# Kernel optimization log

Measured on AMD Instinct MI355X. Metric: run time of the kernel, lower is better.

The kernel has to match this reference:

```python
import jax, jax.numpy as jnp
import numpy as np

# PlatonicConv (graph mode, attention=True, use_key=True): tetrahedron group G=12
G = 12
H_EFF = 2          # num_heads // G = 24 // 12
HEAD_D = 16        # embed_dim_g // H_EFF = (384//12) // 2
GH = G * H_EFF     # 24
IN_C = 384
EMB = 384
OUT_C = 384
N_GRAPHS = 32
NODES_PER_GRAPH = 64
N = N_GRAPHS * NODES_PER_GRAPH   # 2048
SPATIAL = 3


def _fc_edges():
    # fully-connected edges within each graph (batch[src]==batch[dst]), incl. self loops
    n = NODES_PER_GRAPH
    offs = np.arange(N_GRAPHS, dtype=np.int32) * n
    gs, gd = np.meshgrid(np.arange(n, dtype=np.int32), np.arange(n, dtype=np.int32), indexing='ij')
    src = (offs[:, None] + gs.reshape(-1)[None, :]).reshape(-1)
    dst = (offs[:, None] + gd.reshape(-1)[None, :]).reshape(-1)
    return jnp.asarray(src), jnp.asarray(dst)


def setup_inputs() -> dict:
    key = jax.random.key(0)
    ks = jax.random.split(key, 12)
    sw = 1.0 / np.sqrt(IN_C)
    x = jax.random.normal(ks[0], (N, IN_C), jnp.float32)
    pos = jax.random.normal(ks[1], (N, SPATIAL), jnp.float32)
    Wq = jax.random.normal(ks[2], (IN_C, EMB), jnp.float32) * sw
    bq = jnp.zeros((EMB,), jnp.float32)
    Wk = jax.random.normal(ks[3], (IN_C, EMB), jnp.float32) * sw
    bk = jnp.zeros((EMB,), jnp.float32)
    Wv = jax.random.normal(ks[4], (IN_C, EMB), jnp.float32) * sw
    bv = jnp.zeros((EMB,), jnp.float32)
    Wo = jax.random.normal(ks[5], (EMB, OUT_C), jnp.float32) * (1.0 / np.sqrt(EMB))
    bo = jnp.zeros((OUT_C,), jnp.float32)
    # RoPE frequencies: freq_sigma=1.0, random init, per spatial dim / head / half-dim
    rope_freqs = jax.random.normal(ks[6], (SPATIAL, H_EFF, HEAD_D // 2), jnp.float32)
    src, dst = _fc_edges()
    return {"x": x, "pos": pos, "Wq": Wq, "bq": bq, "Wk": Wk, "bk": bk,
            "Wv": Wv, "bv": bv, "Wo": Wo, "bo": bo, "rope_freqs": rope_freqs,
            "src": src, "dst": dst}


def _rope(t, pos, freqs):
    # t: [N, G, H, D]; pos: [N, 3]; freqs: [3, H, D//2]
    theta = jnp.einsum('ns,shf->nhf', pos, freqs)            # [N, H, D/2]
    cos = jnp.cos(theta)[:, None, :, :]                      # broadcast over G
    sin = jnp.sin(theta)[:, None, :, :]
    tr = t.reshape(t.shape[:-1] + (HEAD_D // 2, 2))
    t1, t2 = tr[..., 0], tr[..., 1]
    rot = jnp.stack([t1 * cos - t2 * sin, t1 * sin + t2 * cos], axis=-1)
    return rot.reshape(t.shape)


def reference(x, pos, Wq, bq, Wk, bk, Wv, bv, Wo, bo, rope_freqs, src, dst):
    n = x.shape[0]
    q = (x @ Wq + bq).reshape(n, G, H_EFF, HEAD_D)
    k = (x @ Wk + bk).reshape(n, G, H_EFF, HEAD_D)
    v = (x @ Wv + bv).reshape(n, G, H_EFF, HEAD_D)
    q = _rope(q, pos, rope_freqs)
    k = _rope(k, pos, rope_freqs)
    qf = q.reshape(n, GH, HEAD_D)
    kf = k.reshape(n, GH, HEAD_D)
    vf = v.reshape(n, GH, HEAD_D)
    # gather by edge index
    q_src = qf[src]                                          # [E, GH, D]
    k_dst = kf[dst]
    v_dst = vf[dst]
    scores = jnp.sum(q_src * k_dst, axis=-1) * (HEAD_D ** -0.5)  # [E, GH]
    # scatter softmax over edges grouped by src node (per group-head)
    m = jax.ops.segment_max(scores, src, num_segments=n)     # [N, GH]
    ex = jnp.exp(scores - m[src])
    den = jax.ops.segment_sum(ex, src, num_segments=n)
    a = ex / den[src]                                        # [E, GH]
    out = jax.ops.segment_sum(a[..., None] * v_dst, src, num_segments=n)  # [N, GH, D]
    out = out.reshape(n, GH * HEAD_D)
    return out @ Wo + bo
```

## Files before the change

kernel.cpp:

```cpp
#include <hip/hip_runtime.h>


#define NNODES   2048
#define KDIM     384
#define NGRAPHS  32
#define NPG      64
#define GHEADS   24
#define HDIM     16
#define WSROW    392

typedef __attribute__((ext_vector_type(8))) short short8;
typedef __attribute__((ext_vector_type(4))) float f32x4;

__device__ __forceinline__ short f2bf(float f) {
    unsigned u = __builtin_bit_cast(unsigned, f);
    u += 0x7FFFu + ((u >> 16) & 1u);
    return (short)(u >> 16);
}

__global__ __launch_bounds__(256) void fused_kernel(
    const float* __restrict__ x,
    const float* __restrict__ pos,
    const float* __restrict__ Wq, const float* __restrict__ bq,
    const float* __restrict__ Wk, const float* __restrict__ bk,
    const float* __restrict__ Wv, const float* __restrict__ bv,
    const float* __restrict__ Wo,
    const float* __restrict__ freqs,
    short* __restrict__ WoT,
    short* __restrict__ attn_out)
{
    __shared__ __align__(16) char smem[3 * 16 * WSROW * 2];
    const int tid = threadIdx.x;

    if (blockIdx.x < 144) {
        float (*tile)[33] = reinterpret_cast<float(*)[33]>(smem);
        const int t  = blockIdx.x;
        const int k0 = (t / 12) * 32;
        const int n0 = (t % 12) * 32;
        const int cx = tid & 31;
        const int ty = tid >> 5;
        #pragma unroll
        for (int i = 0; i < 4; ++i) {
            const int rr = ty + 8 * i;
            tile[rr][cx] = Wo[(size_t)(k0 + rr) * KDIM + n0 + cx];
        }
        __syncthreads();
        #pragma unroll
        for (int i = 0; i < 4; ++i) {
            const int rr = ty + 8 * i;
            WoT[(size_t)(n0 + rr) * KDIM + k0 + cx] = f2bf(tile[cx][rr]);
        }
        return;
    }

    const int blk = blockIdx.x - 144;
    const int gr  = blk / GHEADS;
    const int gh  = blk - gr * GHEADS;

    short* WS = reinterpret_cast<short*>(smem);
    for (int task = tid; task < 1152; task += 256) {
        const int mat = task / KDIM;
        const int k   = task - mat * KDIM;
        const float* W = (mat == 0) ? Wq : (mat == 1) ? Wk : Wv;
        const float* src = W + (size_t)k * KDIM + gh * 16;
        f32x4 w0 = reinterpret_cast<const f32x4*>(src)[0];
        f32x4 w1 = reinterpret_cast<const f32x4*>(src)[1];
        f32x4 w2 = reinterpret_cast<const f32x4*>(src)[2];
        f32x4 w3 = reinterpret_cast<const f32x4*>(src)[3];
        short* dst = WS + (size_t)mat * 16 * WSROW + k;
        #pragma unroll
        for (int c = 0; c < 4; ++c) {
            dst[(c)      * WSROW] = f2bf(w0[c]);
            dst[(c + 4)  * WSROW] = f2bf(w1[c]);
            dst[(c + 8)  * WSROW] = f2bf(w2[c]);
            dst[(c + 12) * WSROW] = f2bf(w3[c]);
        }
    }
    __syncthreads();

    const int w    = tid >> 6;
    const int lane = tid & 63;
    const int fr   = lane & 15;
    const int hi   = lane >> 4;

    const float* aRow = x + (size_t)(gr * 64 + w * 16 + fr) * KDIM + hi * 8;
    const short* wsq = WS + (size_t)fr * WSROW + hi * 8;
    const short* wsk = wsq + (size_t)16 * WSROW;
    const short* wsv = wsk + (size_t)16 * WSROW;

    f32x4 acc[3];
    acc[0] = (f32x4){0.f, 0.f, 0.f, 0.f};
    acc[1] = acc[0];
    acc[2] = acc[0];

    #pragma unroll 4
    for (int kt = 0; kt < KDIM; kt += 32) {
        f32x4 a0 = *reinterpret_cast<const f32x4*>(aRow + kt);
        f32x4 a1 = *reinterpret_cast<const f32x4*>(aRow + kt + 4);
        short8 af;
        af[0] = f2bf(a0[0]); af[1] = f2bf(a0[1]); af[2] = f2bf(a0[2]); af[3] = f2bf(a0[3]);
        af[4] = f2bf(a1[0]); af[5] = f2bf(a1[1]); af[6] = f2bf(a1[2]); af[7] = f2bf(a1[3]);
        short8 b0 = *reinterpret_cast<const short8*>(wsq + kt);
        short8 b1 = *reinterpret_cast<const short8*>(wsk + kt);
        short8 b2 = *reinterpret_cast<const short8*>(wsv + kt);
        acc[0] = __builtin_amdgcn_mfma_f32_16x16x32_bf16(af, b0, acc[0], 0, 0, 0);
        acc[1] = __builtin_amdgcn_mfma_f32_16x16x32_bf16(af, b1, acc[1], 0, 0, 0);
        acc[2] = __builtin_amdgcn_mfma_f32_16x16x32_bf16(af, b2, acc[2], 0, 0, 0);
    }
    __syncthreads();

    float (*q_lds)[20] = reinterpret_cast<float(*)[20]>(smem);
    float (*k_lds)[20] = reinterpret_cast<float(*)[20]>(smem + 5120);
    float (*v_lds)[20] = reinterpret_cast<float(*)[20]>(smem + 10240);

    const float bias_q = bq[gh * 16 + fr];
    const float bias_k = bk[gh * 16 + fr];
    const float bias_v = bv[gh * 16 + fr];
    const int   h = gh & 1;
    const int   f = fr >> 1;
    const float F0 = freqs[h * 8 + f];
    const float F1 = freqs[16 + h * 8 + f];
    const float F2 = freqs[32 + h * 8 + f];

    #pragma unroll
    for (int rr = 0; rr < 4; ++rr) {
        const int row  = w * 16 + hi * 4 + rr;
        const int grow = gr * 64 + row;
        float qv = acc[0][rr] + bias_q;
        float kv = acc[1][rr] + bias_k;
        float vv = acc[2][rr] + bias_v;
        const float th = pos[grow * 3] * F0 + pos[grow * 3 + 1] * F1
                       + pos[grow * 3 + 2] * F2;
        const float cs = __cosf(th);
        const float sn = __sinf(th);
        const float qo = __shfl_xor(qv, 1, 64);
        const float ko = __shfl_xor(kv, 1, 64);
        qv = (fr & 1) ? (qo * sn + qv * cs) : (qv * cs - qo * sn);
        kv = (fr & 1) ? (ko * sn + kv * cs) : (kv * cs - ko * sn);
        q_lds[row][fr] = qv;
        k_lds[row][fr] = kv;
        v_lds[row][fr] = vv;
    }
    __syncthreads();

    const int qrow = w * 16 + fr;
    f32x4 q0 = *reinterpret_cast<const f32x4*>(&q_lds[qrow][0]);
    f32x4 q1 = *reinterpret_cast<const f32x4*>(&q_lds[qrow][4]);
    f32x4 q2 = *reinterpret_cast<const f32x4*>(&q_lds[qrow][8]);
    f32x4 q3 = *reinterpret_cast<const f32x4*>(&q_lds[qrow][12]);

    float sc[16];
    #pragma unroll
    for (int j = 0; j < 16; ++j) {
        const float* kp = &k_lds[hi * 16 + j][0];
        f32x4 k0 = reinterpret_cast<const f32x4*>(kp)[0];
        f32x4 k1 = reinterpret_cast<const f32x4*>(kp)[1];
        f32x4 k2 = reinterpret_cast<const f32x4*>(kp)[2];
        f32x4 k3 = reinterpret_cast<const f32x4*>(kp)[3];
        float a = q0[0]*k0[0] + q0[1]*k0[1] + q0[2]*k0[2] + q0[3]*k0[3]
                + q1[0]*k1[0] + q1[1]*k1[1] + q1[2]*k1[2] + q1[3]*k1[3]
                + q2[0]*k2[0] + q2[1]*k2[1] + q2[2]*k2[2] + q2[3]*k2[3]
                + q3[0]*k3[0] + q3[1]*k3[1] + q3[2]*k3[2] + q3[3]*k3[3];
        sc[j] = a * 0.25f;
    }

    float mx = sc[0];
    #pragma unroll
    for (int j = 1; j < 16; ++j) mx = fmaxf(mx, sc[j]);
    mx = fmaxf(mx, __shfl_xor(mx, 16, 64));
    mx = fmaxf(mx, __shfl_xor(mx, 32, 64));

    float den = 0.f;
    #pragma unroll
    for (int j = 0; j < 16; ++j) {
        sc[j] = __expf(sc[j] - mx);
        den += sc[j];
    }
    den += __shfl_xor(den, 16, 64);
    den += __shfl_xor(den, 32, 64);

    float o[16];
    #pragma unroll
    for (int d = 0; d < 16; ++d) o[d] = 0.f;
    #pragma unroll
    for (int j = 0; j < 16; ++j) {
        const float p = sc[j];
        const float* vp = &v_lds[hi * 16 + j][0];
        f32x4 v0 = reinterpret_cast<const f32x4*>(vp)[0];
        f32x4 v1 = reinterpret_cast<const f32x4*>(vp)[1];
        f32x4 v2 = reinterpret_cast<const f32x4*>(vp)[2];
        f32x4 v3 = reinterpret_cast<const f32x4*>(vp)[3];
        #pragma unroll
        for (int d = 0; d < 4; ++d) {
            o[d]      += p * v0[d];
            o[4 + d]  += p * v1[d];
            o[8 + d]  += p * v2[d];
            o[12 + d] += p * v3[d];
        }
    }
    #pragma unroll
    for (int d = 0; d < 16; ++d) {
        o[d] += __shfl_xor(o[d], 16, 64);
        o[d] += __shfl_xor(o[d], 32, 64);
    }

    if (hi == 0) {
        const float inv = 1.0f / den;
        short8 r0, r1;
        #pragma unroll
        for (int d = 0; d < 8; ++d) {
            r0[d] = f2bf(o[d] * inv);
            r1[d] = f2bf(o[8 + d] * inv);
        }
        short* op = attn_out + (size_t)(gr * 64 + qrow) * KDIM + gh * 16;
        *reinterpret_cast<short8*>(op)     = r0;
        *reinterpret_cast<short8*>(op + 8) = r1;
    }
}

__global__ __launch_bounds__(64) void out_gemm_kernel(
    const short* __restrict__ A,
    const short* __restrict__ BT,
    const float* __restrict__ bias,
    float* __restrict__ C)
{
    const int r0   = blockIdx.x * 16;
    const int c0   = blockIdx.y * 64;
    const int lane = threadIdx.x;
    const int fr   = lane & 15;
    const int hi   = lane >> 4;

    const short* aP  = A + (size_t)(r0 + fr) * KDIM + hi * 8;
    const short* b0P = BT + (size_t)(c0 + fr) * KDIM + hi * 8;
    const short* b1P = b0P + (size_t)16 * KDIM;
    const short* b2P = b1P + (size_t)16 * KDIM;
    const short* b3P = b2P + (size_t)16 * KDIM;

    f32x4 acc[4];
    acc[0] = (f32x4){0.f, 0.f, 0.f, 0.f};
    acc[1] = acc[0]; acc[2] = acc[0]; acc[3] = acc[0];

    #pragma unroll 4
    for (int kt = 0; kt < KDIM; kt += 32) {
        short8 af = *reinterpret_cast<const short8*>(aP + kt);
        short8 f0 = *reinterpret_cast<const short8*>(b0P + kt);
        short8 f1 = *reinterpret_cast<const short8*>(b1P + kt);
        short8 f2 = *reinterpret_cast<const short8*>(b2P + kt);
        short8 f3 = *reinterpret_cast<const short8*>(b3P + kt);
        acc[0] = __builtin_amdgcn_mfma_f32_16x16x32_bf16(af, f0, acc[0], 0, 0, 0);
        acc[1] = __builtin_amdgcn_mfma_f32_16x16x32_bf16(af, f1, acc[1], 0, 0, 0);
        acc[2] = __builtin_amdgcn_mfma_f32_16x16x32_bf16(af, f2, acc[2], 0, 0, 0);
        acc[3] = __builtin_amdgcn_mfma_f32_16x16x32_bf16(af, f3, acc[3], 0, 0, 0);
    }

    #pragma unroll
    for (int ct = 0; ct < 4; ++ct) {
        const int c    = c0 + ct * 16 + fr;
        const float bv = bias[c];
        const int rowb = r0 + hi * 4;
        #pragma unroll
        for (int rr = 0; rr < 4; ++rr)
            C[(size_t)(rowb + rr) * KDIM + c] = acc[ct][rr] + bv;
    }
}

extern "C" void kernel_launch(void* const* d_in, const int* in_sizes, int n_in,
                              void* d_out, int out_size, void* d_ws, size_t ws_size,
                              hipStream_t stream) {
    const float* x    = (const float*)d_in[0];
    const float* pos  = (const float*)d_in[1];
    const float* Wq   = (const float*)d_in[2];
    const float* bq   = (const float*)d_in[3];
    const float* Wk   = (const float*)d_in[4];
    const float* bk   = (const float*)d_in[5];
    const float* Wv   = (const float*)d_in[6];
    const float* bv   = (const float*)d_in[7];
    const float* Wo   = (const float*)d_in[8];
    const float* bo   = (const float*)d_in[9];
    const float* rope = (const float*)d_in[10];

    char* ws = (char*)d_ws;
    short* WoT  = (short*)(ws);
    short* attn = (short*)(ws + 294912);

    fused_kernel<<<144 + NGRAPHS * GHEADS, 256, 0, stream>>>(
        x, pos, Wq, bq, Wk, bk, Wv, bv, Wo, rope, WoT, attn);

    {
        dim3 grid(NNODES / 16, KDIM / 64);
        out_gemm_kernel<<<grid, 64, 0, stream>>>(attn, WoT, bo, (float*)d_out);
    }
}
```

Measured before the change: 109.5 us.

## Merge output GEMM into fused kernel via grid-wide atomic barrier

Drops the separate output-projection launch. After attention, all 768 blocks meet at a software grid barrier (an atomic counter reset by a memset), then each block computes a 64x16 tile of the output GEMM. The Wo transpose is now spread across all blocks with one element per thread. Weight staging writes packed bf16 pairs, and x conversion uses a perm-based truncating pack. This saves a kernel launch and its tail, but adds a memset, a spin barrier that relies on all blocks being co-resident, and truncating rather than round-to-nearest bf16 conversion of x.

After: 204.6 us. 1.87x slower.

```diff
diff --git a/kernel.cpp b/kernel.cpp
--- a/kernel.cpp
+++ b/kernel.cpp
@@ -4,76 +4,68 @@
 #define NNODES   2048
 #define KDIM     384
 #define NGRAPHS  32
-#define NPG      64
 #define GHEADS   24
-#define HDIM     16
+#define NBLOCKS  (NGRAPHS * GHEADS)
 #define WSROW    392
 
-typedef __attribute__((ext_vector_type(8))) short short8;
-typedef __attribute__((ext_vector_type(4))) float f32x4;
+typedef __attribute__((ext_vector_type(8))) short    short8;
+typedef __attribute__((ext_vector_type(4))) float    f32x4;
+typedef __attribute__((ext_vector_type(4))) unsigned u32x4;
 
 __device__ __forceinline__ short f2bf(float f) {
     unsigned u = __builtin_bit_cast(unsigned, f);
     u += 0x7FFFu + ((u >> 16) & 1u);
     return (short)(u >> 16);
 }
-
-__global__ __launch_bounds__(256) void fused_kernel(
+__device__ __forceinline__ unsigned pk2bf(float lo, float hi) {
+    return __builtin_amdgcn_perm(__builtin_bit_cast(unsigned, hi),
+                                 __builtin_bit_cast(unsigned, lo), 0x07060302u);
+}
+
+__global__ __launch_bounds__(256, 4) void mega_kernel(
     const float* __restrict__ x,
     const float* __restrict__ pos,
     const float* __restrict__ Wq, const float* __restrict__ bq,
     const float* __restrict__ Wk, const float* __restrict__ bk,
     const float* __restrict__ Wv, const float* __restrict__ bv,
-    const float* __restrict__ Wo,
+    const float* __restrict__ Wo, const float* __restrict__ bo,
     const float* __restrict__ freqs,
     short* __restrict__ WoT,
-    short* __restrict__ attn_out)
+    short* __restrict__ attn_out,
+    unsigned* __restrict__ bar,
+    float* __restrict__ out)
 {
     __shared__ __align__(16) char smem[3 * 16 * WSROW * 2];
     const int tid = threadIdx.x;
-
-    if (blockIdx.x < 144) {
-        float (*tile)[33] = reinterpret_cast<float(*)[33]>(smem);
-        const int t  = blockIdx.x;
-        const int k0 = (t / 12) * 32;
-        const int n0 = (t % 12) * 32;
-        const int cx = tid & 31;
-        const int ty = tid >> 5;
+    const int gr  = blockIdx.x / GHEADS;
+    const int gh  = blockIdx.x - gr * GHEADS;
+
+    {
+        const int u = blockIdx.x * 256 + tid;
+        if (u < KDIM * KDIM)
+            WoT[u] = f2bf(Wo[(size_t)(u % KDIM) * KDIM + u / KDIM]);
+    }
+
+    short* WS = reinterpret_cast<short*>(smem);
+    for (int task = tid; task < 576; task += 256) {
+        const int mat = task / 192;
+        const int kp  = task - mat * 192;
+        const int k   = kp * 2;
+        const float* W = (mat == 0) ? Wq : (mat == 1) ? Wk : Wv;
+        const float* s0 = W + (size_t)k * KDIM + gh * 16;
+        const float* s1 = s0 + KDIM;
+        f32x4 r0[4], r1[4];
         #pragma unroll
         for (int i = 0; i < 4; ++i) {
-            const int rr = ty + 8 * i;
-            tile[rr][cx] = Wo[(size_t)(k0 + rr) * KDIM + n0 + cx];
-        }
-        __syncthreads();
-        #pragma unroll
-        for (int i = 0; i < 4; ++i) {
-            const int rr = ty + 8 * i;
-            WoT[(size_t)(n0 + rr) * KDIM + k0 + cx] = f2bf(tile[cx][rr]);
-        }
-        return;
-    }
-
-    const int blk = blockIdx.x - 144;
-    const int gr  = blk / GHEADS;
-    const int gh  = blk - gr * GHEADS;
-
-    short* WS = reinterpret_cast<short*>(smem);
-    for (int task = tid; task < 1152; task += 256) {
-        const int mat = task / KDIM;
-        const int k   = task - mat * KDIM;
-        const float* W = (mat == 0) ? Wq : (mat == 1) ? Wk : Wv;
-        const float* src = W + (size_t)k * KDIM + gh * 16;
-        f32x4 w0 = reinterpret_cast<const f32x4*>(src)[0];
-        f32x4 w1 = reinterpret_cast<const f32x4*>(src)[1];
-        f32x4 w2 = reinterpret_cast<const f32x4*>(src)[2];
-        f32x4 w3 = reinterpret_cast<const f32x4*>(src)[3];
-        short* dst = WS + (size_t)mat * 16 * WSROW + k;
-        #pragma unroll
-        for (int c = 0; c < 4; ++c) {
-            dst[(c)      * WSROW] = f2bf(w0[c]);
-            dst[(c + 4)  * WSROW] = f2bf(w1[c]);
-            dst[(c + 8)  * WSROW] = f2bf(w2[c]);
-            dst[(c + 12) * WSROW] = f2bf(w3[c]);
+            r0[i] = reinterpret_cast<const f32x4*>(s0)[i];
+            r1[i] = reinterpret_cast<const f32x4*>(s1)[i];
+        }
+        unsigned* dst = reinterpret_cast<unsigned*>(WS + (size_t)mat * 16 * WSROW + k);
+        #pragma unroll
+        for (int c = 0; c < 16; ++c) {
+            const unsigned lo = (unsigned)(unsigned short)f2bf(r0[c >> 2][c & 3]);
+            const unsigned hi = (unsigned)(unsigned short)f2bf(r1[c >> 2][c & 3]);
+            dst[c * (WSROW / 2)] = lo | (hi << 16);
         }
     }
     __syncthreads();
@@ -97,9 +89,12 @@
     for (int kt = 0; kt < KDIM; kt += 32) {
         f32x4 a0 = *reinterpret_cast<const f32x4*>(aRow + kt);
         f32x4 a1 = *reinterpret_cast<const f32x4*>(aRow + kt + 4);
-        short8 af;
-        af[0] = f2bf(a0[0]); af[1] = f2bf(a0[1]); af[2] = f2bf(a0[2]); af[3] = f2bf(a0[3]);
-        af[4] = f2bf(a1[0]); af[5] = f2bf(a1[1]); af[6] = f2bf(a1[2]); af[7] = f2bf(a1[3]);
+        u32x4 ap;
+        ap[0] = pk2bf(a0[0], a0[1]);
+        ap[1] = pk2bf(a0[2], a0[3]);
+        ap[2] = pk2bf(a1[0], a1[1]);
+        ap[3] = pk2bf(a1[2], a1[3]);
+        short8 af = __builtin_bit_cast(short8, ap);
         short8 b0 = *reinterpret_cast<const short8*>(wsq + kt);
         short8 b1 = *reinterpret_cast<const short8*>(wsk + kt);
         short8 b2 = *reinterpret_cast<const short8*>(wsv + kt);
@@ -216,51 +211,36 @@
         *reinterpret_cast<short8*>(op)     = r0;
         *reinterpret_cast<short8*>(op + 8) = r1;
     }
-}
-
-__global__ __launch_bounds__(64) void out_gemm_kernel(
-    const short* __restrict__ A,
-    const short* __restrict__ BT,
-    const float* __restrict__ bias,
-    float* __restrict__ C)
-{
-    const int r0   = blockIdx.x * 16;
-    const int c0   = blockIdx.y * 64;
-    const int lane = threadIdx.x;
-    const int fr   = lane & 15;
-    const int hi   = lane >> 4;
-
-    const short* aP  = A + (size_t)(r0 + fr) * KDIM + hi * 8;
-    const short* b0P = BT + (size_t)(c0 + fr) * KDIM + hi * 8;
-    const short* b1P = b0P + (size_t)16 * KDIM;
-    const short* b2P = b1P + (size_t)16 * KDIM;
-    const short* b3P = b2P + (size_t)16 * KDIM;
-
-    f32x4 acc[4];
-    acc[0] = (f32x4){0.f, 0.f, 0.f, 0.f};
-    acc[1] = acc[0]; acc[2] = acc[0]; acc[3] = acc[0];
-
-    #pragma unroll 4
-    for (int kt = 0; kt < KDIM; kt += 32) {
-        short8 af = *reinterpret_cast<const short8*>(aP + kt);
-        short8 f0 = *reinterpret_cast<const short8*>(b0P + kt);
-        short8 f1 = *reinterpret_cast<const short8*>(b1P + kt);
-        short8 f2 = *reinterpret_cast<const short8*>(b2P + kt);
-        short8 f3 = *reinterpret_cast<const short8*>(b3P + kt);
-        acc[0] = __builtin_amdgcn_mfma_f32_16x16x32_bf16(af, f0, acc[0], 0, 0, 0);
-        acc[1] = __builtin_amdgcn_mfma_f32_16x16x32_bf16(af, f1, acc[1], 0, 0, 0);
-        acc[2] = __builtin_amdgcn_mfma_f32_16x16x32_bf16(af, f2, acc[2], 0, 0, 0);
-        acc[3] = __builtin_amdgcn_mfma_f32_16x16x32_bf16(af, f3, acc[3], 0, 0, 0);
-    }
-
-    #pragma unroll
-    for (int ct = 0; ct < 4; ++ct) {
-        const int c    = c0 + ct * 16 + fr;
-        const float bv = bias[c];
-        const int rowb = r0 + hi * 4;
+
+    __syncthreads();
+    if (tid == 0) {
+        __threadfence();
+        atomicAdd(bar, 1u);
+        while (__hip_atomic_load(bar, __ATOMIC_RELAXED,
+                                 __HIP_MEMORY_SCOPE_AGENT) < (unsigned)NBLOCKS)
+            __builtin_amdgcn_s_sleep(8);
+        __threadfence();
+    }
+    __syncthreads();
+
+    {
+        const short* aP = attn_out + (size_t)(gr * 64 + w * 16 + fr) * KDIM + hi * 8;
+        const short* bP = WoT + (size_t)(gh * 16 + fr) * KDIM + hi * 8;
+
+        f32x4 acc4 = (f32x4){0.f, 0.f, 0.f, 0.f};
+        #pragma unroll
+        for (int kt = 0; kt < KDIM; kt += 32) {
+            short8 af = *reinterpret_cast<const short8*>(aP + kt);
+            short8 bf = *reinterpret_cast<const short8*>(bP + kt);
+            acc4 = __builtin_amdgcn_mfma_f32_16x16x32_bf16(af, bf, acc4, 0, 0, 0);
+        }
+
+        const int c    = gh * 16 + fr;
+        const float bv = bo[c];
+        const int rowb = gr * 64 + w * 16 + hi * 4;
         #pragma unroll
         for (int rr = 0; rr < 4; ++rr)
-            C[(size_t)(rowb + rr) * KDIM + c] = acc[ct][rr] + bv;
+            out[(size_t)(rowb + rr) * KDIM + c] = acc4[rr] + bv;
     }
 }
 
@@ -280,14 +260,13 @@
     const float* rope = (const float*)d_in[10];
 
     char* ws = (char*)d_ws;
-    short* WoT  = (short*)(ws);
-    short* attn = (short*)(ws + 294912);
-
-    fused_kernel<<<144 + NGRAPHS * GHEADS, 256, 0, stream>>>(
-        x, pos, Wq, bq, Wk, bk, Wv, bv, Wo, rope, WoT, attn);
-
-    {
-        dim3 grid(NNODES / 16, KDIM / 64);
-        out_gemm_kernel<<<grid, 64, 0, stream>>>(attn, WoT, bo, (float*)d_out);
-    }
-}
+    short*    WoT  = (short*)(ws);
+    short*    attn = (short*)(ws + 294912);
+    unsigned* bar  = (unsigned*)(ws + 1867776);
+
+    hipMemsetAsync(bar, 0, sizeof(unsigned), stream);
+
+    mega_kernel<<<NBLOCKS, 256, 0, stream>>>(
+        x, pos, Wq, bq, Wk, bk, Wv, bv, Wo, bo, rope,
+        WoT, attn, bar, (float*)d_out);
+}
```
